# Kernel tuning notes

Measured on AMD Instinct MI355X. Metric: run time of the kernel, lower is better.

## Reference

```python
import jax, jax.numpy as jnp
import numpy as np

B, N1, N2, C1, C2 = 8, 8192, 2048, 128, 256
O1, O2 = 256, 256
IN_CH = C2 + C1  # 384
BN_EPS = 1e-5


def setup_inputs() -> dict:
    key = jax.random.key(0)
    ks = jax.random.split(key, 6)
    return {
        "xyz1": jax.random.normal(ks[0], (B, N1, 3), dtype=jnp.float32),
        "xyz2": jax.random.normal(ks[1], (B, N2, 3), dtype=jnp.float32),
        "feats1": jax.random.normal(ks[2], (B, C1, N1), dtype=jnp.float32),
        "feats2": jax.random.normal(ks[3], (B, C2, N2), dtype=jnp.float32),
        "W1": jax.random.normal(ks[4], (O1, IN_CH), dtype=jnp.float32) * 0.02,
        "b1": jnp.zeros((O1,), jnp.float32),
        "g1": jnp.ones((O1,), jnp.float32),
        "be1": jnp.zeros((O1,), jnp.float32),
        "W2": jax.random.normal(ks[5], (O2, O1), dtype=jnp.float32) * 0.02,
        "b2": jnp.zeros((O2,), jnp.float32),
        "g2": jnp.ones((O2,), jnp.float32),
        "be2": jnp.zeros((O2,), jnp.float32),
    }


def _bn(x, g, b):
    # eval-mode BatchNorm1d with init running stats (mean=0, var=1)
    return g[None, :, None] * x * (1.0 / jnp.sqrt(1.0 + BN_EPS)) + b[None, :, None]


def reference(xyz1, xyz2, feats1, feats2, W1, b1, g1, be1, W2, b2, g2, be2):
    # pairwise Euclidean distances (B, N1, N2), torch.cdist equivalent
    d2 = (jnp.sum(xyz1 * xyz1, -1)[:, :, None]
          + jnp.sum(xyz2 * xyz2, -1)[:, None, :]
          - 2.0 * jnp.einsum('bnc,bmc->bnm', xyz1, xyz2))
    d = jnp.sqrt(jnp.maximum(d2, 0.0))
    # 3 nearest neighbors (smallest distances)
    neg_d, idx = jax.lax.top_k(-d, 3)          # idx: (B, N1, 3)
    knn_d = jnp.maximum(-neg_d, 1e-8)
    w = 1.0 / knn_d
    w = w / jnp.sum(w, -1, keepdims=True)       # (B, N1, 3)
    # gather neighbor features: feats2 (B,C2,N2) -> (B,N2,C2) -> (B,N1,3,C2)
    f2p = jnp.swapaxes(feats2, 1, 2)
    neigh = f2p[jnp.arange(B)[:, None, None], idx]
    out = jnp.einsum('bnk,bnkc->bcn', w, neigh)  # (B, C2, N1)
    out = jnp.concatenate([out, feats1], axis=1)  # (B, C2+C1, N1)
    # Conv1d(k=1) + BN + ReLU, twice
    h = jax.nn.relu(_bn(jnp.einsum('oc,bcn->bon', W1, out) + b1[None, :, None], g1, be1))
    h = jax.nn.relu(_bn(jnp.einsum('oc,bcn->bon', W2, h) + b2[None, :, None], g2, be2))
    return h
```

## Files before the change

kernel.cpp:

```cpp
#include <hip/hip_runtime.h>

typedef __attribute__((ext_vector_type(8))) short bf16x8;
typedef __attribute__((ext_vector_type(4))) float f32x4;
typedef __attribute__((ext_vector_type(4))) unsigned short u16x4;

__device__ __forceinline__ unsigned short f2bf(float f) {
  unsigned u = __float_as_uint(f);
  u += 0x7FFFu + ((u >> 16) & 1u);
  return (unsigned short)(u >> 16);
}

__global__ __launch_bounds__(256) void prep(
    const float* __restrict__ f1, const float* __restrict__ f2,
    const float* __restrict__ W1, const float* __restrict__ W2,
    short* __restrict__ ft1, float* __restrict__ f2t,
    short* __restrict__ wpk1, short* __restrict__ wpk2) {
  __shared__ float tile[64][65];
  const int bx = blockIdx.x, b = blockIdx.y, t = threadIdx.x;
  const int tj = t & 63, tr = t >> 6;
  if (bx < 128) {
    int j0 = (bx & 31) * 64, c0 = (bx >> 5) * 64;
#pragma unroll
    for (int p = 0; p < 16; ++p) {
      int ci = p * 4 + tr;
      tile[ci][tj] = f2[(size_t)(b * 256 + c0 + ci) * 2048 + j0 + tj];
    }
    __syncthreads();
#pragma unroll
    for (int p = 0; p < 16; ++p) {
      int jr = p * 4 + tr;
      f2t[(size_t)(b * 2048 + j0 + jr) * 256 + c0 + tj] = tile[tj][jr];
    }
  } else if (bx < 384) {
    int i = bx - 128;
    int j0 = (i & 127) * 64, c0 = (i >> 7) * 64;
#pragma unroll
    for (int p = 0; p < 16; ++p) {
      int ci = p * 4 + tr;
      tile[ci][tj] = f1[(size_t)(b * 128 + c0 + ci) * 8192 + j0 + tj];
    }
    __syncthreads();
#pragma unroll
    for (int p = 0; p < 16; ++p) {
      int jr = p * 4 + tr;
      ft1[((size_t)b * 8192 + j0 + jr) * 128 + c0 + tj] = (short)f2bf(tile[tj][jr]);
    }
  } else {
    int pb = (bx - 384) * 8 + b;
    int id = pb * 256 + t;
    if (id < 98304) {
      int j = id & 7, lane = (id >> 3) & 63, mt = (id >> 9) & 15, kt = id >> 13;
      int o = mt * 16 + (lane & 15);
      int c = kt * 32 + ((lane >> 4) & 3) * 8 + j;
      wpk1[id] = (short)f2bf(W1[o * 384 + c]);
    } else {
      int f = id - 98304;
      int j = f & 7, lane = (f >> 3) & 63, mt = (f >> 9) & 15, kt = f >> 13;
      int o = mt * 16 + (lane & 15);
      int c = kt * 32 + ((lane >> 4) & 3) * 8 + j;
      wpk2[f] = (short)f2bf(W2[o * 256 + c]);
    }
  }
}

__device__ __forceinline__ void merge44d(double a0, double a1, double a2, double a3,
                                         double c0, double c1, double c2, double c3,
                                         double& o0, double& o1, double& o2, double& o3) {
#define POP(OD)                                                           \
  {                                                                       \
    bool s = a0 < c0;                                                     \
    OD = s ? a0 : c0;                                                     \
    double sa0 = s ? a1 : a0, sa1 = s ? a2 : a1, sa2 = s ? a3 : a2;       \
    double sc0 = s ? c0 : c1, sc1 = s ? c1 : c2, sc2 = s ? c2 : c3;       \
    a3 = s ? 1e300 : a3; c3 = s ? c3 : 1e300;                             \
    a0 = sa0; a1 = sa1; a2 = sa2; c0 = sc0; c1 = sc1; c2 = sc2;           \
  }
  POP(o0) POP(o1) POP(o2) POP(o3)
#undef POP
}

__global__ __launch_bounds__(512) void fused(
    const float* __restrict__ xyz1, const float* __restrict__ xyz2,
    const float* __restrict__ f2t, const short* __restrict__ ft1,
    const short* __restrict__ wpk1, const short* __restrict__ wpk2,
    const float* __restrict__ b1, const float* __restrict__ g1, const float* __restrict__ be1,
    const float* __restrict__ b2, const float* __restrict__ g2, const float* __restrict__ be2,
    float* __restrict__ out) {
  __shared__ __align__(16) char R1[32768];
  __shared__ __align__(16) double T4[2048];
  __shared__ float W3s[192];
  __shared__ int   ID3s[192];

  const int t = threadIdx.x, lane = t & 63, wid = t >> 6;
  const int b = blockIdx.y, n0 = blockIdx.x * 64;
  const int l15 = lane & 15, l4 = lane >> 4;

  {
    float4* pkB = (float4*)R1;
    for (int j = t; j < 2048; j += 512) {
      const float* p = xyz2 + ((size_t)b * 2048 + j) * 3;
      float px = p[0], py = p[1], pz = p[2];
      float s2 = __fadd_rn(__fadd_rn(__fmul_rn(px, px), __fmul_rn(py, py)), __fmul_rn(pz, pz));
      pkB[j] = make_float4(px, py, pz, s2);
    }
  }
  const int qq = t & 63, seg = wid;
  float qx, qy, qz, s1;
  {
    const float* p = xyz1 + ((size_t)b * 8192 + n0 + qq) * 3;
    qx = p[0]; qy = p[1]; qz = p[2];
    s1 = __fadd_rn(__fadd_rn(__fmul_rn(qx, qx), __fmul_rn(qy, qy)), __fmul_rn(qz, qz));
  }
  __syncthreads();

  {
    double k0 = 1e300, k1 = 1e300, k2 = 1e300, k3 = 1e300;
    const float4* pkB = (const float4*)R1;
    int jb = seg * 256;
    double jd = (double)jb;
#pragma unroll 4
    for (int j = jb; j < jb + 256; ++j) {
      float4 P = pkB[j];
      float dot = __fadd_rn(__fadd_rn(__fmul_rn(qx, P.x), __fmul_rn(qy, P.y)), __fmul_rn(qz, P.z));
      float d2 = __fsub_rn(__fadd_rn(s1, P.w), __fadd_rn(dot, dot));
      float dc = fmaxf(d2, 0.0f);
      double K = fma((double)__float_as_uint(dc), 2048.0, jd);
      jd += 1.0;
      double t0 = fmax(k0, K); k0 = fmin(k0, K);
      double t1 = fmax(k1, t0); k1 = fmin(k1, t0);
      double t2 = fmax(k2, t1); k2 = fmin(k2, t1);
      k3 = fmin(k3, t2);
    }
    T4[0 * 512 + t] = k0; T4[1 * 512 + t] = k1;
    T4[2 * 512 + t] = k2; T4[3 * 512 + t] = k3;
  }
  __syncthreads();

  if (t < 64) {
    double l[8][4];
#pragma unroll
    for (int k = 0; k < 8; ++k)
#pragma unroll
      for (int s = 0; s < 4; ++s) l[k][s] = T4[s * 512 + k * 64 + t];
    double m01[4], m23[4], m45[4], m67[4], ma[4], mb[4], mf[4];
    merge44d(l[0][0], l[0][1], l[0][2], l[0][3], l[1][0], l[1][1], l[1][2], l[1][3],
             m01[0], m01[1], m01[2], m01[3]);
    merge44d(l[2][0], l[2][1], l[2][2], l[2][3], l[3][0], l[3][1], l[3][2], l[3][3],
             m23[0], m23[1], m23[2], m23[3]);
    merge44d(l[4][0], l[4][1], l[4][2], l[4][3], l[5][0], l[5][1], l[5][2], l[5][3],
             m45[0], m45[1], m45[2], m45[3]);
    merge44d(l[6][0], l[6][1], l[6][2], l[6][3], l[7][0], l[7][1], l[7][2], l[7][3],
             m67[0], m67[1], m67[2], m67[3]);
    merge44d(m01[0], m01[1], m01[2], m01[3], m23[0], m23[1], m23[2], m23[3],
             ma[0], ma[1], ma[2], ma[3]);
    merge44d(m45[0], m45[1], m45[2], m45[3], m67[0], m67[1], m67[2], m67[3],
             mb[0], mb[1], mb[2], mb[3]);
    merge44d(ma[0], ma[1], ma[2], ma[3], mb[0], mb[1], mb[2], mb[3],
             mf[0], mf[1], mf[2], mf[3]);
    float e[4]; int ji[4];
#pragma unroll
    for (int s = 0; s < 4; ++s) {
      double qd = mf[s] * (1.0 / 2048.0);
      double qf = trunc(qd);
      double jd = fma(-qf, 2048.0, mf[s]);
      ji[s] = (int)jd;
      unsigned dcb = (unsigned)qf;
      e[s] = __fsqrt_rn(__uint_as_float(dcb));
    }
#define SW(X, Y)                                                          \
  {                                                                       \
    bool sw = (e[X] > e[Y]) || ((e[X] == e[Y]) && (ji[X] > ji[Y]));       \
    float td = e[X]; int ti = ji[X];                                      \
    e[X] = sw ? e[Y] : e[X]; ji[X] = sw ? ji[Y] : ji[X];                  \
    e[Y] = sw ? td : e[Y];   ji[Y] = sw ? ti : ji[Y];                     \
  }
    SW(0, 1) SW(1, 2) SW(2, 3) SW(0, 1) SW(1, 2) SW(0, 1)
#undef SW
    float k0 = fmaxf(e[0], 1e-8f), k1 = fmaxf(e[1], 1e-8f), k2 = fmaxf(e[2], 1e-8f);
    float u0 = 1.0f / k0, u1 = 1.0f / k1, u2 = 1.0f / k2;
    float ss = __fadd_rn(__fadd_rn(u0, u1), u2);
    W3s[t * 3 + 0] = u0 / ss; W3s[t * 3 + 1] = u1 / ss; W3s[t * 3 + 2] = u2 / ss;
    ID3s[t * 3 + 0] = ji[0]; ID3s[t * 3 + 1] = ji[1]; ID3s[t * 3 + 2] = ji[2];
  }
  __syncthreads();

  {
    const int c = t & 255, half = t >> 8;
    const size_t f2b = (size_t)b * 2048 * 256;
#pragma unroll 2
    for (int qi = 0; qi < 32; ++qi) {
      int q = half * 32 + qi;
      int j0 = ID3s[q * 3 + 0], j1 = ID3s[q * 3 + 1], j2 = ID3s[q * 3 + 2];
      float W0 = W3s[q * 3 + 0], W1v = W3s[q * 3 + 1], W2v = W3s[q * 3 + 2];
      float v0 = f2t[f2b + (size_t)j0 * 256 + c];
      float v1 = f2t[f2b + (size_t)j1 * 256 + c];
      float v2 = f2t[f2b + (size_t)j2 * 256 + c];
      float v = W0 * v0 + W1v * v1 + W2v * v2;
      int addr = (q * 512 + c * 2) ^ ((q & 7) << 4);
      *(unsigned short*)(R1 + addr) = f2bf(v);
    }
  }
  __syncthreads();

  f32x4 acc[2][4];
#pragma unroll
  for (int m = 0; m < 2; ++m)
#pragma unroll
    for (int n = 0; n < 4; ++n) acc[m][n] = (f32x4){0.f, 0.f, 0.f, 0.f};

#pragma unroll
  for (int kt = 0; kt < 8; ++kt) {
    bf16x8 a[2], bb[4];
#pragma unroll
    for (int m = 0; m < 2; ++m)
      a[m] = *(const bf16x8*)(wpk1 + ((size_t)(kt * 16 + wid * 2 + m) * 64 + lane) * 8);
#pragma unroll
    for (int nt = 0; nt < 4; ++nt) {
      int q = nt * 16 + l15;
      int addr = q * 512 + ((kt * 64 + l4 * 16) ^ ((q & 7) << 4));
      bb[nt] = *(const bf16x8*)(R1 + addr);
    }
#pragma unroll
    for (int m = 0; m < 2; ++m)
#pragma unroll
      for (int nt = 0; nt < 4; ++nt)
        acc[m][nt] = __builtin_amdgcn_mfma_f32_16x16x32_bf16(a[m], bb[nt], acc[m][nt], 0, 0, 0);
  }
#pragma unroll
  for (int kt = 8; kt < 12; ++kt) {
    bf16x8 a[2], bb[4];
#pragma unroll
    for (int m = 0; m < 2; ++m)
      a[m] = *(const bf16x8*)(wpk1 + ((size_t)(kt * 16 + wid * 2 + m) * 64 + lane) * 8);
#pragma unroll
    for (int nt = 0; nt < 4; ++nt)
      bb[nt] = *(const bf16x8*)(ft1 + ((size_t)b * 8192 + n0 + nt * 16 + l15) * 128 +
                                (kt - 8) * 32 + l4 * 8);
#pragma unroll
    for (int m = 0; m < 2; ++m)
#pragma unroll
      for (int nt = 0; nt < 4; ++nt)
        acc[m][nt] = __builtin_amdgcn_mfma_f32_16x16x32_bf16(a[m], bb[nt], acc[m][nt], 0, 0, 0);
  }
  __syncthreads();

  const float BNINV = 0.99999500003749972f;
#pragma unroll
  for (int m = 0; m < 2; ++m) {
    int cb = wid * 32 + m * 16 + l4 * 4;
    float gv[4], bv[4], ev[4];
#pragma unroll
    for (int r = 0; r < 4; ++r) {
      gv[r] = g1[cb + r] * BNINV; bv[r] = b1[cb + r]; ev[r] = be1[cb + r];
    }
#pragma unroll
    for (int nt = 0; nt < 4; ++nt) {
      int q = nt * 16 + l15;
      u16x4 pk4;
#pragma unroll
      for (int r = 0; r < 4; ++r)
        pk4[r] = f2bf(fmaxf((acc[m][nt][r] + bv[r]) * gv[r] + ev[r], 0.0f));
      *(u16x4*)(R1 + ((q * 512 + cb * 2) ^ ((q & 7) << 4))) = pk4;
    }
  }
  __syncthreads();

#pragma unroll
  for (int m = 0; m < 2; ++m)
#pragma unroll
    for (int n = 0; n < 4; ++n) acc[m][n] = (f32x4){0.f, 0.f, 0.f, 0.f};
#pragma unroll
  for (int kt = 0; kt < 8; ++kt) {
    bf16x8 a[2], bb[4];
#pragma unroll
    for (int m = 0; m < 2; ++m)
      a[m] = *(const bf16x8*)(wpk2 + ((size_t)(kt * 16 + wid * 2 + m) * 64 + lane) * 8);
#pragma unroll
    for (int nt = 0; nt < 4; ++nt) {
      int q = nt * 16 + l15;
      int addr = q * 512 + ((kt * 64 + l4 * 16) ^ ((q & 7) << 4));
      bb[nt] = *(const bf16x8*)(R1 + addr);
    }
#pragma unroll
    for (int m = 0; m < 2; ++m)
#pragma unroll
      for (int nt = 0; nt < 4; ++nt)
        acc[m][nt] = __builtin_amdgcn_mfma_f32_16x16x32_bf16(a[m], bb[nt], acc[m][nt], 0, 0, 0);
  }

#pragma unroll
  for (int m = 0; m < 2; ++m) {
    int ob = wid * 32 + m * 16 + l4 * 4;
    float gv[4], bv[4], ev[4];
#pragma unroll
    for (int r = 0; r < 4; ++r) {
      gv[r] = g2[ob + r] * BNINV; bv[r] = b2[ob + r]; ev[r] = be2[ob + r];
    }
#pragma unroll
    for (int nt = 0; nt < 4; ++nt) {
      int nn = n0 + nt * 16 + l15;
#pragma unroll
      for (int r = 0; r < 4; ++r)
        out[((size_t)b * 256 + ob + r) * 8192 + nn] =
            fmaxf((acc[m][nt][r] + bv[r]) * gv[r] + ev[r], 0.0f);
    }
  }
}

extern "C" void kernel_launch(void* const* d_in, const int* in_sizes, int n_in,
                              void* d_out, int out_size, void* d_ws, size_t ws_size,
                              hipStream_t stream) {
  (void)in_sizes; (void)n_in; (void)out_size; (void)ws_size;
  const float* xyz1   = (const float*)d_in[0];
  const float* xyz2   = (const float*)d_in[1];
  const float* feats1 = (const float*)d_in[2];
  const float* feats2 = (const float*)d_in[3];
  const float* W1  = (const float*)d_in[4];
  const float* b1  = (const float*)d_in[5];
  const float* g1  = (const float*)d_in[6];
  const float* be1 = (const float*)d_in[7];
  const float* W2  = (const float*)d_in[8];
  const float* b2  = (const float*)d_in[9];
  const float* g2  = (const float*)d_in[10];
  const float* be2 = (const float*)d_in[11];
  float* out = (float*)d_out;

  char* ws = (char*)d_ws;
  short* wpk1 = (short*)(ws);
  short* wpk2 = (short*)(ws + 196608);
  float* f2t  = (float*)(ws + 327680);
  short* ft1  = (short*)(ws + 17104896);

  prep<<<dim3(464, 8), 256, 0, stream>>>(feats1, feats2, W1, W2, ft1, f2t, wpk1, wpk2);
  fused<<<dim3(128, 8), 512, 0, stream>>>(xyz1, xyz2, f2t, ft1, wpk1, wpk2,
                                          b1, g1, be1, b2, g2, be2, out);
}
```

Baseline: 231.5 us.

## Store feats2 as bf16, precompute packed xyz2, use 32-bit KNN keys with tree merge

The prep kernel now writes the transposed feats2 as bf16 instead of fp32, which halves the gather traffic. It also precomputes packed xyz2 with squared norms into global memory, so the fused kernel reads that directly instead of staging it in shared memory. The KNN inner loop swaps the double-precision packed key insertion for 32-bit unsigned distance and index registers, and the 8-way merge becomes a parallel tree across waves. Shared memory is cut, a launch-bounds occupancy hint is added, and the grid is flattened with the batch index interleaved. In exchange, feats2 is rounded to bf16 before interpolation, which adds precision error.

```diff
diff --git a/kernel.cpp b/kernel.cpp
--- a/kernel.cpp
+++ b/kernel.cpp
@@ -12,14 +12,17 @@
 
 __global__ __launch_bounds__(256) void prep(
     const float* __restrict__ f1, const float* __restrict__ f2,
+    const float* __restrict__ xyz2,
     const float* __restrict__ W1, const float* __restrict__ W2,
-    short* __restrict__ ft1, float* __restrict__ f2t,
-    short* __restrict__ wpk1, short* __restrict__ wpk2) {
+    short* __restrict__ ft1, unsigned short* __restrict__ ft2,
+    short* __restrict__ wpk1, short* __restrict__ wpk2,
+    float4* __restrict__ xyz2s) {
   __shared__ float tile[64][65];
-  const int bx = blockIdx.x, b = blockIdx.y, t = threadIdx.x;
+  const int bid = blockIdx.x, t = threadIdx.x;
   const int tj = t & 63, tr = t >> 6;
-  if (bx < 128) {
-    int j0 = (bx & 31) * 64, c0 = (bx >> 5) * 64;
+  if (bid < 1024) {
+    int b = bid & 7, i = bid >> 3;
+    int j0 = (i & 31) * 64, c0 = (i >> 5) * 64;
 #pragma unroll
     for (int p = 0; p < 16; ++p) {
       int ci = p * 4 + tr;
@@ -29,11 +32,12 @@
 #pragma unroll
     for (int p = 0; p < 16; ++p) {
       int jr = p * 4 + tr;
-      f2t[(size_t)(b * 2048 + j0 + jr) * 256 + c0 + tj] = tile[tj][jr];
-    }
-  } else if (bx < 384) {
-    int i = bx - 128;
-    int j0 = (i & 127) * 64, c0 = (i >> 7) * 64;
+      ft2[(size_t)(b * 2048 + j0 + jr) * 256 + c0 + tj] = f2bf(tile[tj][jr]);
+    }
+  } else if (bid < 3072) {
+    int i = bid - 1024;
+    int b = i & 7, ii = i >> 3;
+    int j0 = (ii & 127) * 64, c0 = (ii >> 7) * 64;
 #pragma unroll
     for (int p = 0; p < 16; ++p) {
       int ci = p * 4 + tr;
@@ -46,19 +50,26 @@
       ft1[((size_t)b * 8192 + j0 + jr) * 128 + c0 + tj] = (short)f2bf(tile[tj][jr]);
     }
   } else {
-    int pb = (bx - 384) * 8 + b;
-    int id = pb * 256 + t;
+    int id = (bid - 3072) * 256 + t;
     if (id < 98304) {
       int j = id & 7, lane = (id >> 3) & 63, mt = (id >> 9) & 15, kt = id >> 13;
       int o = mt * 16 + (lane & 15);
       int c = kt * 32 + ((lane >> 4) & 3) * 8 + j;
       wpk1[id] = (short)f2bf(W1[o * 384 + c]);
-    } else {
+    } else if (id < 163840) {
       int f = id - 98304;
       int j = f & 7, lane = (f >> 3) & 63, mt = (f >> 9) & 15, kt = f >> 13;
       int o = mt * 16 + (lane & 15);
       int c = kt * 32 + ((lane >> 4) & 3) * 8 + j;
       wpk2[f] = (short)f2bf(W2[o * 256 + c]);
+    } else {
+      int p = id - 163840;
+      int b = p >> 11, j = p & 2047;
+      const float* q = xyz2 + (size_t)(b * 2048 + j) * 3;
+      float px = q[0], py = q[1], pz = q[2];
+      float s2 = __fadd_rn(__fadd_rn(__fmul_rn(px, px), __fmul_rn(py, py)),
+                           __fmul_rn(pz, pz));
+      xyz2s[b * 2048 + j] = make_float4(px, py, pz, s2);
     }
   }
 }
@@ -79,84 +90,98 @@
 #undef POP
 }
 
-__global__ __launch_bounds__(512) void fused(
-    const float* __restrict__ xyz1, const float* __restrict__ xyz2,
-    const float* __restrict__ f2t, const short* __restrict__ ft1,
+__global__ __launch_bounds__(512, 8) void fused(
+    const float* __restrict__ xyz1, const float4* __restrict__ xyz2s,
+    const unsigned short* __restrict__ ft2, const short* __restrict__ ft1,
     const short* __restrict__ wpk1, const short* __restrict__ wpk2,
     const float* __restrict__ b1, const float* __restrict__ g1, const float* __restrict__ be1,
     const float* __restrict__ b2, const float* __restrict__ g2, const float* __restrict__ be2,
     float* __restrict__ out) {
-  __shared__ __align__(16) char R1[32768];
-  __shared__ __align__(16) double T4[2048];
-  __shared__ float W3s[192];
-  __shared__ int   ID3s[192];
+  __shared__ __align__(16) char XH[32768];
+  __shared__ __align__(16) double T4[1024];
+  float* W3s = (float*)((char*)T4 + 6144);
+  int*  ID3s = (int*)((char*)T4 + 6912);
 
   const int t = threadIdx.x, lane = t & 63, wid = t >> 6;
-  const int b = blockIdx.y, n0 = blockIdx.x * 64;
+  const int blk = blockIdx.x;
+  const int b = blk & 7, n0 = (blk >> 3) * 64;
   const int l15 = lane & 15, l4 = lane >> 4;
 
-  {
-    float4* pkB = (float4*)R1;
-    for (int j = t; j < 2048; j += 512) {
-      const float* p = xyz2 + ((size_t)b * 2048 + j) * 3;
-      float px = p[0], py = p[1], pz = p[2];
-      float s2 = __fadd_rn(__fadd_rn(__fmul_rn(px, px), __fmul_rn(py, py)), __fmul_rn(pz, pz));
-      pkB[j] = make_float4(px, py, pz, s2);
-    }
-  }
-  const int qq = t & 63, seg = wid;
   float qx, qy, qz, s1;
   {
-    const float* p = xyz1 + ((size_t)b * 8192 + n0 + qq) * 3;
+    const float* p = xyz1 + ((size_t)b * 8192 + n0 + lane) * 3;
     qx = p[0]; qy = p[1]; qz = p[2];
     s1 = __fadd_rn(__fadd_rn(__fmul_rn(qx, qx), __fmul_rn(qy, qy)), __fmul_rn(qz, qz));
   }
-  __syncthreads();
-
+
+  unsigned k0 = 0xFFFFFFFFu, k1 = 0xFFFFFFFFu, k2 = 0xFFFFFFFFu, k3 = 0xFFFFFFFFu;
+  unsigned i0 = 0, i1 = 0, i2 = 0, i3 = 0;
   {
-    double k0 = 1e300, k1 = 1e300, k2 = 1e300, k3 = 1e300;
-    const float4* pkB = (const float4*)R1;
-    int jb = seg * 256;
-    double jd = (double)jb;
+    const int jb = __builtin_amdgcn_readfirstlane(wid * 256);
+    const float4* __restrict__ pk = xyz2s + (size_t)b * 2048;
 #pragma unroll 4
-    for (int j = jb; j < jb + 256; ++j) {
-      float4 P = pkB[j];
-      float dot = __fadd_rn(__fadd_rn(__fmul_rn(qx, P.x), __fmul_rn(qy, P.y)), __fmul_rn(qz, P.z));
+    for (int jo = 0; jo < 256; ++jo) {
+      int j = jb + jo;
+      float4 P = pk[j];
+      float dot = __fadd_rn(__fadd_rn(__fmul_rn(qx, P.x), __fmul_rn(qy, P.y)),
+                            __fmul_rn(qz, P.z));
       float d2 = __fsub_rn(__fadd_rn(s1, P.w), __fadd_rn(dot, dot));
-      float dc = fmaxf(d2, 0.0f);
-      double K = fma((double)__float_as_uint(dc), 2048.0, jd);
-      jd += 1.0;
-      double t0 = fmax(k0, K); k0 = fmin(k0, K);
-      double t1 = fmax(k1, t0); k1 = fmin(k1, t0);
-      double t2 = fmax(k2, t1); k2 = fmin(k2, t1);
-      k3 = fmin(k3, t2);
-    }
-    T4[0 * 512 + t] = k0; T4[1 * 512 + t] = k1;
-    T4[2 * 512 + t] = k2; T4[3 * 512 + t] = k3;
-  }
-  __syncthreads();
-
-  if (t < 64) {
-    double l[8][4];
-#pragma unroll
-    for (int k = 0; k < 8; ++k)
-#pragma unroll
-      for (int s = 0; s < 4; ++s) l[k][s] = T4[s * 512 + k * 64 + t];
-    double m01[4], m23[4], m45[4], m67[4], ma[4], mb[4], mf[4];
-    merge44d(l[0][0], l[0][1], l[0][2], l[0][3], l[1][0], l[1][1], l[1][2], l[1][3],
-             m01[0], m01[1], m01[2], m01[3]);
-    merge44d(l[2][0], l[2][1], l[2][2], l[2][3], l[3][0], l[3][1], l[3][2], l[3][3],
-             m23[0], m23[1], m23[2], m23[3]);
-    merge44d(l[4][0], l[4][1], l[4][2], l[4][3], l[5][0], l[5][1], l[5][2], l[5][3],
-             m45[0], m45[1], m45[2], m45[3]);
-    merge44d(l[6][0], l[6][1], l[6][2], l[6][3], l[7][0], l[7][1], l[7][2], l[7][3],
-             m67[0], m67[1], m67[2], m67[3]);
-    merge44d(m01[0], m01[1], m01[2], m01[3], m23[0], m23[1], m23[2], m23[3],
-             ma[0], ma[1], ma[2], ma[3]);
-    merge44d(m45[0], m45[1], m45[2], m45[3], m67[0], m67[1], m67[2], m67[3],
-             mb[0], mb[1], mb[2], mb[3]);
-    merge44d(ma[0], ma[1], ma[2], ma[3], mb[0], mb[1], mb[2], mb[3],
-             mf[0], mf[1], mf[2], mf[3]);
+      unsigned K = __float_as_uint(fmaxf(d2, 0.0f));
+      bool l0 = K < k0, l1 = K < k1, l2 = K < k2, l3 = K < k3;
+      unsigned nk0 = min(k0, K);
+      unsigned nk1 = min(max(K, k0), k1);
+      unsigned nk2 = min(max(K, k1), k2);
+      unsigned nk3 = min(max(K, k2), k3);
+      unsigned uj = (unsigned)j;
+      unsigned ni0 = l0 ? uj : i0;
+      unsigned ni1 = l0 ? i0 : (l1 ? uj : i1);
+      unsigned ni2 = l1 ? i1 : (l2 ? uj : i2);
+      unsigned ni3 = l2 ? i2 : (l3 ? uj : i3);
+      k0 = nk0; k1 = nk1; k2 = nk2; k3 = nk3;
+      i0 = ni0; i1 = ni1; i2 = ni2; i3 = ni3;
+    }
+  }
+  double key0 = fma((double)k0, 2048.0, (double)i0);
+  double key1 = fma((double)k1, 2048.0, (double)i1);
+  double key2 = fma((double)k2, 2048.0, (double)i2);
+  double key3 = fma((double)k3, 2048.0, (double)i3);
+
+  if (wid >= 4) {
+    int w = wid - 4;
+    T4[0 * 256 + w * 64 + lane] = key0; T4[1 * 256 + w * 64 + lane] = key1;
+    T4[2 * 256 + w * 64 + lane] = key2; T4[3 * 256 + w * 64 + lane] = key3;
+  }
+  __syncthreads();
+  double m10 = 0, m11 = 0, m12 = 0, m13 = 0;
+  if (wid < 4) {
+    double p0 = T4[0 * 256 + wid * 64 + lane], p1 = T4[1 * 256 + wid * 64 + lane];
+    double p2 = T4[2 * 256 + wid * 64 + lane], p3 = T4[3 * 256 + wid * 64 + lane];
+    merge44d(key0, key1, key2, key3, p0, p1, p2, p3, m10, m11, m12, m13);
+  }
+  __syncthreads();
+  if (wid == 2 || wid == 3) {
+    int w = wid - 2;
+    T4[0 * 128 + w * 64 + lane] = m10; T4[1 * 128 + w * 64 + lane] = m11;
+    T4[2 * 128 + w * 64 + lane] = m12; T4[3 * 128 + w * 64 + lane] = m13;
+  }
+  __syncthreads();
+  double m20 = 0, m21 = 0, m22 = 0, m23 = 0;
+  if (wid < 2) {
+    double p0 = T4[0 * 128 + wid * 64 + lane], p1 = T4[1 * 128 + wid * 64 + lane];
+    double p2 = T4[2 * 128 + wid * 64 + lane], p3 = T4[3 * 128 + wid * 64 + lane];
+    merge44d(m10, m11, m12, m13, p0, p1, p2, p3, m20, m21, m22, m23);
+  }
+  __syncthreads();
+  if (wid == 1) {
+    T4[0 * 64 + lane] = m20; T4[1 * 64 + lane] = m21;
+    T4[2 * 64 + lane] = m22; T4[3 * 64 + lane] = m23;
+  }
+  __syncthreads();
+  if (wid == 0) {
+    double p0 = T4[0 * 64 + lane], p1 = T4[1 * 64 + lane];
+    double p2 = T4[2 * 64 + lane], p3 = T4[3 * 64 + lane];
+    double mf[4];
+    merge44d(m20, m21, m22, m23, p0, p1, p2, p3, mf[0], mf[1], mf[2], mf[3]);
     float e[4]; int ji[4];
 #pragma unroll
     for (int s = 0; s < 4; ++s) {
@@ -164,8 +189,7 @@
       double qf = trunc(qd);
       double jd = fma(-qf, 2048.0, mf[s]);
       ji[s] = (int)jd;
-      unsigned dcb = (unsigned)qf;
-      e[s] = __fsqrt_rn(__uint_as_float(dcb));
+      e[s] = __fsqrt_rn(__uint_as_float((unsigned)qf));
     }
 #define SW(X, Y)                                                          \
   {                                                                       \
@@ -176,11 +200,11 @@
   }
     SW(0, 1) SW(1, 2) SW(2, 3) SW(0, 1) SW(1, 2) SW(0, 1)
 #undef SW
-    float k0 = fmaxf(e[0], 1e-8f), k1 = fmaxf(e[1], 1e-8f), k2 = fmaxf(e[2], 1e-8f);
-    float u0 = 1.0f / k0, u1 = 1.0f / k1, u2 = 1.0f / k2;
+    float c0 = fmaxf(e[0], 1e-8f), c1 = fmaxf(e[1], 1e-8f), c2 = fmaxf(e[2], 1e-8f);
+    float u0 = 1.0f / c0, u1 = 1.0f / c1, u2 = 1.0f / c2;
     float ss = __fadd_rn(__fadd_rn(u0, u1), u2);
-    W3s[t * 3 + 0] = u0 / ss; W3s[t * 3 + 1] = u1 / ss; W3s[t * 3 + 2] = u2 / ss;
-    ID3s[t * 3 + 0] = ji[0]; ID3s[t * 3 + 1] = ji[1]; ID3s[t * 3 + 2] = ji[2];
+    W3s[lane * 3 + 0] = u0 / ss; W3s[lane * 3 + 1] = u1 / ss; W3s[lane * 3 + 2] = u2 / ss;
+    ID3s[lane * 3 + 0] = ji[0]; ID3s[lane * 3 + 1] = ji[1]; ID3s[lane * 3 + 2] = ji[2];
   }
   __syncthreads();
 
@@ -192,12 +216,12 @@
       int q = half * 32 + qi;
       int j0 = ID3s[q * 3 + 0], j1 = ID3s[q * 3 + 1], j2 = ID3s[q * 3 + 2];
       float W0 = W3s[q * 3 + 0], W1v = W3s[q * 3 + 1], W2v = W3s[q * 3 + 2];
-      float v0 = f2t[f2b + (size_t)j0 * 256 + c];
-      float v1 = f2t[f2b + (size_t)j1 * 256 + c];
-      float v2 = f2t[f2b + (size_t)j2 * 256 + c];
+      float v0 = __uint_as_float((unsigned)ft2[f2b + (size_t)j0 * 256 + c] << 16);
+      float v1 = __uint_as_float((unsigned)ft2[f2b + (size_t)j1 * 256 + c] << 16);
+      float v2 = __uint_as_float((unsigned)ft2[f2b + (size_t)j2 * 256 + c] << 16);
       float v = W0 * v0 + W1v * v1 + W2v * v2;
       int addr = (q * 512 + c * 2) ^ ((q & 7) << 4);
-      *(unsigned short*)(R1 + addr) = f2bf(v);
+      *(unsigned short*)(XH + addr) = f2bf(v);
     }
   }
   __syncthreads();
@@ -218,7 +242,7 @@
     for (int nt = 0; nt < 4; ++nt) {
       int q = nt * 16 + l15;
       int addr = q * 512 + ((kt * 64 + l4 * 16) ^ ((q & 7) << 4));
-      bb[nt] = *(const bf16x8*)(R1 + addr);
+      bb[nt] = *(const bf16x8*)(XH + addr);
     }
 #pragma unroll
     for (int m = 0; m < 2; ++m)
@@ -260,7 +284,7 @@
 #pragma unroll
       for (int r = 0; r < 4; ++r)
         pk4[r] = f2bf(fmaxf((acc[m][nt][r] + bv[r]) * gv[r] + ev[r], 0.0f));
-      *(u16x4*)(R1 + ((q * 512 + cb * 2) ^ ((q & 7) << 4))) = pk4;
+      *(u16x4*)(XH + ((q * 512 + cb * 2) ^ ((q & 7) << 4))) = pk4;
     }
   }
   __syncthreads();
@@ -279,7 +303,7 @@
     for (int nt = 0; nt < 4; ++nt) {
       int q = nt * 16 + l15;
       int addr = q * 512 + ((kt * 64 + l4 * 16) ^ ((q & 7) << 4));
-      bb[nt] = *(const bf16x8*)(R1 + addr);
+      bb[nt] = *(const bf16x8*)(XH + addr);
     }
 #pragma unroll
     for (int m = 0; m < 2; ++m)
@@ -326,12 +350,14 @@
   float* out = (float*)d_out;
 
   char* ws = (char*)d_ws;
-  short* wpk1 = (short*)(ws);
-  short* wpk2 = (short*)(ws + 196608);
-  float* f2t  = (float*)(ws + 327680);
-  short* ft1  = (short*)(ws + 17104896);
-
-  prep<<<dim3(464, 8), 256, 0, stream>>>(feats1, feats2, W1, W2, ft1, f2t, wpk1, wpk2);
-  fused<<<dim3(128, 8), 512, 0, stream>>>(xyz1, xyz2, f2t, ft1, wpk1, wpk2,
-                                          b1, g1, be1, b2, g2, be2, out);
-}
+  short*          wpk1  = (short*)(ws);
+  short*          wpk2  = (short*)(ws + 196608);
+  float4*         xyz2s = (float4*)(ws + 327680);
+  unsigned short* ft2   = (unsigned short*)(ws + 589824);
+  short*          ft1   = (short*)(ws + 8978432);
+
+  prep<<<3776, 256, 0, stream>>>(feats1, feats2, xyz2, W1, W2,
+                                 ft1, ft2, wpk1, wpk2, xyz2s);
+  fused<<<1024, 512, 0, stream>>>(xyz1, xyz2s, ft2, ft1, wpk1, wpk2,
+                                  b1, g1, be1, b2, g2, be2, out);
+}
```

Result: slower. 267.0 us (+15.4%).
